# Kernel optimization log

Measured on AMD Instinct MI355X. Metric: run time of the kernel, lower is better.

Reference implementation:

```python
import jax, jax.numpy as jnp
import numpy as np
import math

NUM_HEADS = 12
HEAD_DIM = 64
DEGREE = 3
POLY_DIM = HEAD_DIM * (DEGREE + 1)  # 256
MEM_HID = 512
HIDDEN = 768


def setup_inputs() -> dict:
    key = jax.random.key(0)
    ks = jax.random.split(key, 6)
    B, S = 4, 2048
    hidden_states = jax.random.normal(ks[0], (B, S, HIDDEN), dtype=jnp.float32)
    # q projection weight stored (in, out) so y = x @ Wq
    Wq = jax.random.normal(ks[1], (HIDDEN, HIDDEN), dtype=jnp.float32) / np.sqrt(HIDDEN)
    # polynomial coefficients initialized to 1/i!
    coeffs = jnp.array([1.0 / math.factorial(i) for i in range(DEGREE + 1)], dtype=jnp.float32)
    # deep memory MLP: Linear(poly_dim->mem_hid) + ReLU + Linear(mem_hid->poly_dim)
    W1 = jax.random.normal(ks[2], (POLY_DIM, MEM_HID), dtype=jnp.float32) / np.sqrt(POLY_DIM)
    b1 = jnp.zeros((MEM_HID,), dtype=jnp.float32)
    W2 = jax.random.normal(ks[3], (MEM_HID, POLY_DIM), dtype=jnp.float32) / np.sqrt(MEM_HID)
    b2 = jnp.zeros((POLY_DIM,), dtype=jnp.float32)
    return {"hidden_states": hidden_states, "Wq": Wq, "coeffs": coeffs,
            "W1": W1, "b1": b1, "W2": W2, "b2": b2}


def _poly_map(x, coeffs):
    # x: [..., head_dim] -> [..., head_dim*(degree+1)]
    xs = jnp.clip(x, -10.0, 10.0)
    feats = [coeffs[0] * jnp.ones_like(x)]
    for i in range(1, DEGREE + 1):
        feats.append(jnp.clip(coeffs[i] * xs ** i, -1e6, 1e6))
    return jnp.concatenate(feats, axis=-1)


def reference(hidden_states, Wq, coeffs, W1, b1, W2, b2):
    B, S, H = hidden_states.shape
    # q projection -> [B, S, nh, hd]
    q = (hidden_states @ Wq).reshape(B, S, NUM_HEADS, HEAD_DIM)
    # polynomial feature expansion -> [B, S, nh, poly_dim]
    poly_q = _poly_map(q, coeffs)
    flat = poly_q.reshape(-1, POLY_DIM)  # [B*S*nh, poly_dim]
    # deep memory MLP (test-time memory read)
    h = jax.nn.relu(flat @ W1 + b1)
    mem = h @ W2 + b2  # [B*S*nh, poly_dim]
    # slice first head_dim dims, fold heads back into hidden
    out = mem[:, :HEAD_DIM].reshape(B, S, NUM_HEADS * HEAD_DIM)
    return out
```

## Files before the change

### kernel.cpp

```cpp
#include <hip/hip_runtime.h>


typedef unsigned short u16;
typedef __attribute__((ext_vector_type(8))) short short8;
typedef __attribute__((ext_vector_type(4))) float f32x4;
typedef __attribute__((ext_vector_type(4))) u16 u16x4;

__device__ __forceinline__ u16 f2bf(float f) {
    unsigned u = __builtin_bit_cast(unsigned, f);
    u += 0x7FFFu + ((u >> 16) & 1u);
    return (u16)(u >> 16);
}

__device__ __forceinline__ unsigned cvtpk_bf16(float lo, float hi) {
    unsigned r;
    asm("v_cvt_pk_bf16_f32 %0, %1, %2" : "=v"(r) : "v"(lo), "v"(hi));
    return r;
}

__device__ __forceinline__ void gl2lds16(const void* g, void* l) {
    __builtin_amdgcn_global_load_lds(
        (const __attribute__((address_space(1))) unsigned int*)g,
        (__attribute__((address_space(3))) unsigned int*)l, 16, 0, 0);
}

#define WAIT_VM_LGKM_BAR(N) \
    asm volatile("s_waitcnt vmcnt(" #N ") lgkmcnt(0)\n\ts_barrier" ::: "memory")
#define WAIT_LGKM_BAR() \
    asm volatile("s_waitcnt lgkmcnt(0)\n\ts_barrier" ::: "memory")

__global__ __launch_bounds__(256)
void prep(const float* __restrict__ X, u16* __restrict__ Xb,
          const float* __restrict__ Wq, u16* __restrict__ Wqb,
          const float* __restrict__ W1, u16* __restrict__ W1b,
          const float* __restrict__ W2, u16* __restrict__ W2b,
          const float* __restrict__ b1, const float* __restrict__ coeffs,
          float* __restrict__ b1e)
{
    __shared__ float t[32][33];
    const int b = blockIdx.x, tid = threadIdx.x;

    if (b < 6144) {
        const int i = b * 256 + tid;
        float4 v = reinterpret_cast<const float4*>(X)[i];
        u16x4 o = {f2bf(v.x), f2bf(v.y), f2bf(v.z), f2bf(v.w)};
        reinterpret_cast<u16x4*>(Xb)[i] = o;
    } else if (b < 6880) {
        const float* in; u16* out; int R, Cin, bx, by;
        int lb = b - 6144;
        if (lb < 576)      { in = Wq; out = Wqb; R = 768; Cin = 768; bx = lb % 24; by = lb / 24; }
        else if (lb < 704) { lb -= 576; in = W1; out = W1b; R = 256; Cin = 512; bx = lb % 16; by = lb / 16; }
        else               { lb -= 704; in = W2; out = W2b; R = 512; Cin = 256; bx = lb % 2;  by = lb / 2; }
        const int c0 = bx * 32, r0 = by * 32;
        const int tx = tid & 31, ty = tid >> 5;
        #pragma unroll
        for (int j = 0; j < 32; j += 8)
            t[ty + j][tx] = in[(size_t)(r0 + ty + j) * Cin + c0 + tx];
        __syncthreads();
        #pragma unroll
        for (int j = 0; j < 32; j += 8)
            out[(size_t)(c0 + ty + j) * R + r0 + tx] = f2bf(t[tx][ty + j]);
    } else {
        const int n = (b - 6880) * 256 + tid;
        float s = 0.f;
        #pragma unroll 8
        for (int k = 0; k < 64; ++k) s += W1[k * 512 + n];
        b1e[n] = b1[n] + coeffs[0] * s;
    }
}


__global__ __launch_bounds__(256, 2)
void fused(const u16* __restrict__ Xb, const u16* __restrict__ Wqb,
           const float* __restrict__ coeffs,
           const u16* __restrict__ W1t, const float* __restrict__ b1e,
           const u16* __restrict__ W2t, const float* __restrict__ b2,
           float* __restrict__ out)
{
    __shared__ u16 shm[37888];

    const int tid = threadIdx.x;
    const int w = tid >> 6, lane = tid & 63;
    const int lrow = lane >> 2, lslot = lane & 3;
    const int m16 = lane & 15, quad = lane >> 4;
    const int w0 = w & 1, w1 = w >> 1;
    const int tok0 = blockIdx.x * 64;
    const int bn = blockIdx.y * 128;
    const int h0 = blockIdx.y * 2;

    const float c1 = coeffs[1], c2 = coeffs[2], c3 = coeffs[3];

    u16* const qt    = shm;
    u16* const ring1 = shm + 9216;
    u16* const ring2 = shm + 9216;
    u16* const HsB   = shm + 21504;

    f32x4 acc[4][2];
    #pragma unroll
    for (int i = 0; i < 4; ++i)
        #pragma unroll
        for (int j = 0; j < 2; ++j)
            acc[i][j] = (f32x4){0.f, 0.f, 0.f, 0.f};

    auto stage1 = [&](int slot, int g) {
        const int k0 = g * 32;
        u16* Xs = ring1 + slot * 6144;
        u16* Ws = Xs + 2048;
        {
            const int row = w * 16 + lrow;
            const int cc = lslot ^ ((row >> 2) & 3);
            gl2lds16(Xb + (size_t)(tok0 + row) * 768 + k0 + cc * 8, &Xs[row * 32 + lslot * 8]);
        }
        #pragma unroll
        for (int i = 0; i < 2; ++i) {
            const int row = (w * 2 + i) * 16 + lrow;
            const int cc = lslot ^ ((row >> 2) & 3);
            gl2lds16(Wqb + (size_t)(bn + row) * 768 + k0 + cc * 8, &Ws[row * 32 + lslot * 8]);
        }
    };

    stage1(0, 0);
    stage1(1, 1);

    #pragma unroll 1
    for (int g = 0; g < 24; ++g) {
        WAIT_VM_LGKM_BAR(3);
        stage1((g + 2) % 3, (g + 2 <= 23) ? g + 2 : 23);
        const u16* Xs = ring1 + (g % 3) * 6144;
        const u16* Ws = Xs + 2048;
        short8 a[4], b[2];
        #pragma unroll
        for (int i = 0; i < 4; ++i) {
            const int row = w0 * 64 + i * 16 + m16;
            const int ss = quad ^ ((row >> 2) & 3);
            a[i] = *reinterpret_cast<const short8*>(&Ws[row * 32 + ss * 8]);
        }
        #pragma unroll
        for (int j = 0; j < 2; ++j) {
            const int row = w1 * 32 + j * 16 + m16;
            const int ss = quad ^ ((row >> 2) & 3);
            b[j] = *reinterpret_cast<const short8*>(&Xs[row * 32 + ss * 8]);
        }
        __builtin_amdgcn_s_setprio(1);
        #pragma unroll
        for (int i = 0; i < 4; ++i)
            #pragma unroll
            for (int j = 0; j < 2; ++j)
                acc[i][j] = __builtin_amdgcn_mfma_f32_16x16x32_bf16(a[i], b[j], acc[i][j], 0, 0, 0);
        __builtin_amdgcn_s_setprio(0);
    }

    asm volatile("s_waitcnt vmcnt(0) lgkmcnt(0)\n\ts_barrier" ::: "memory");

    #pragma unroll
    for (int i = 0; i < 4; ++i) {
        const int d0 = i * 16 + quad * 4;
        #pragma unroll
        for (int j = 0; j < 2; ++j) {
            const int l = (w1 * 32 + j * 16 + m16) * 2 + w0;
            float x0 = fminf(fmaxf(acc[i][j][0], -10.f), 10.f);
            float x1 = fminf(fmaxf(acc[i][j][1], -10.f), 10.f);
            float x2 = fminf(fmaxf(acc[i][j][2], -10.f), 10.f);
            float x3 = fminf(fmaxf(acc[i][j][3], -10.f), 10.f);
            uint2 v;
            v.x = cvtpk_bf16(x0, x1);
            v.y = cvtpk_bf16(x2, x3);
            *reinterpret_cast<uint2*>(&qt[l * 72 + d0]) = v;
        }
    }

    auto stage2 = [&](int slot, int g) {
        const int s = g / 6, c = g % 6;
        u16* W1s = ring2 + slot * 4096;
        #pragma unroll
        for (int i = 0; i < 2; ++i) {
            const int row = (w * 2 + i) * 16 + lrow;
            const int cc = lslot ^ ((row >> 2) & 3);
            gl2lds16(W1t + (size_t)(s * 128 + row) * 256 + 64 + c * 32 + cc * 8,
                     &W1s[row * 32 + lslot * 8]);
        }
    };
    auto stage2c = [&](int slot, int gg) {
        if (gg <= 23) stage2(slot, gg);
        else if (gg == 24) stage2(slot, 23);
    };

    short8 b3s[4][2];
    auto loadW2 = [&](int s) {
        #pragma unroll
        for (int c = 0; c < 4; ++c)
            #pragma unroll
            for (int j = 0; j < 2; ++j)
                b3s[c][j] = *reinterpret_cast<const short8*>(
                    W2t + (size_t)(w1 * 32 + j * 16 + m16) * 512 + s * 128 + c * 32 + quad * 8);
    };

    f32x4 accO[4][2];
    #pragma unroll
    for (int i = 0; i < 4; ++i)
        #pragma unroll
        for (int j = 0; j < 2; ++j)
            accO[i][j] = (f32x4){0.f, 0.f, 0.f, 0.f};

    stage2(0, 0);
    stage2(1, 1);

    #pragma unroll 1
    for (int s = 0; s < 4; ++s) {
        f32x4 accH[4][4];
        #pragma unroll
        for (int i = 0; i < 4; ++i)
            #pragma unroll
            for (int j = 0; j < 4; ++j)
                accH[i][j] = (f32x4){0.f, 0.f, 0.f, 0.f};

        auto computeH = [&](int slot, int c) {
            const u16* W1s = ring2 + slot * 4096;
            short8 af[4], bf[4];
            #pragma unroll
            for (int i = 0; i < 4; ++i) {
                const int row = w0 * 64 + i * 16 + m16;
                const int ss = quad ^ ((row >> 2) & 3);
                af[i] = *reinterpret_cast<const short8*>(&W1s[row * 32 + ss * 8]);
            }
            #pragma unroll
            for (int j = 0; j < 4; ++j) {
                const int row = w1 * 64 + j * 16 + m16;
                short8 qv = *reinterpret_cast<const short8*>(
                    &qt[row * 72 + (c & 1) * 32 + quad * 8]);
                float y[8];
                #pragma unroll
                for (int e = 0; e < 8; ++e) {
                    float x = __builtin_bit_cast(float, ((unsigned)(u16)qv[e]) << 16);
                    if (c < 2)      y[e] = c1 * x;
                    else if (c < 4) y[e] = c2 * (x * x);
                    else            y[e] = (c3 * (x * x)) * x;
                }
                uint4 pk;
                pk.x = cvtpk_bf16(y[0], y[1]);
                pk.y = cvtpk_bf16(y[2], y[3]);
                pk.z = cvtpk_bf16(y[4], y[5]);
                pk.w = cvtpk_bf16(y[6], y[7]);
                bf[j] = __builtin_bit_cast(short8, pk);
            }
            __builtin_amdgcn_s_setprio(1);
            #pragma unroll
            for (int i = 0; i < 4; ++i)
                #pragma unroll
                for (int j = 0; j < 4; ++j)
                    accH[i][j] = __builtin_amdgcn_mfma_f32_16x16x32_bf16(af[i], bf[j], accH[i][j], 0, 0, 0);
            __builtin_amdgcn_s_setprio(0);
        };

        const int g0 = s * 6;
        WAIT_VM_LGKM_BAR(2);  stage2c(2, g0 + 2); loadW2(s); computeH(0, 0);
        WAIT_VM_LGKM_BAR(10); stage2c(0, g0 + 3);            computeH(1, 1);
        WAIT_VM_LGKM_BAR(10); stage2c(1, g0 + 4);            computeH(2, 2);
        WAIT_VM_LGKM_BAR(2);  stage2c(2, g0 + 5);            computeH(0, 3);
        WAIT_VM_LGKM_BAR(2);  stage2c(0, g0 + 6);            computeH(1, 4);
        WAIT_VM_LGKM_BAR(2);  stage2c(1, g0 + 7);            computeH(2, 5);

        #pragma unroll
        for (int i = 0; i < 4; ++i) {
            const int lb = w0 * 64 + i * 16 + quad * 4;
            const f32x4 bv = *reinterpret_cast<const f32x4*>(&b1e[s * 128 + lb]);
            const int hc = lb >> 5;
            #pragma unroll
            for (int j = 0; j < 4; ++j) {
                const int tc = w1 * 64 + j * 16 + m16;
                const float h0v = fmaxf(accH[i][j][0] + bv[0], 0.f);
                const float h1v = fmaxf(accH[i][j][1] + bv[1], 0.f);
                const float h2v = fmaxf(accH[i][j][2] + bv[2], 0.f);
                const float h3v = fmaxf(accH[i][j][3] + bv[3], 0.f);
                uint2 v;
                v.x = cvtpk_bf16(h0v, h1v);
                v.y = cvtpk_bf16(h2v, h3v);
                const int sl = ((lb >> 3) & 3) ^ ((tc >> 2) & 3);
                *reinterpret_cast<uint2*>(&HsB[hc * 4096 + tc * 32 + sl * 8 + (lb & 7)]) = v;
            }
        }

        WAIT_LGKM_BAR();

        __builtin_amdgcn_s_setprio(1);
        #pragma unroll
        for (int c = 0; c < 4; ++c) {
            short8 a3[4];
            #pragma unroll
            for (int i = 0; i < 4; ++i) {
                const int tr = w0 * 64 + i * 16 + m16;
                const int ss = quad ^ ((tr >> 2) & 3);
                a3[i] = *reinterpret_cast<const short8*>(&HsB[c * 4096 + tr * 32 + ss * 8]);
            }
            #pragma unroll
            for (int i = 0; i < 4; ++i)
                #pragma unroll
                for (int j = 0; j < 2; ++j)
                    accO[i][j] = __builtin_amdgcn_mfma_f32_16x16x32_bf16(a3[i], b3s[c][j], accO[i][j], 0, 0, 0);
        }
        __builtin_amdgcn_s_setprio(0);
    }

    asm volatile("s_waitcnt vmcnt(0)" ::: "memory");

    #pragma unroll
    for (int j = 0; j < 2; ++j) {
        const int col = w1 * 32 + j * 16 + m16;
        const float bv = b2[col];
        #pragma unroll
        for (int i = 0; i < 4; ++i) {
            #pragma unroll
            for (int r = 0; r < 4; ++r) {
                const int l = w0 * 64 + i * 16 + quad * 4 + r;
                const size_t orow = (size_t)(tok0 + (l >> 1)) * 12 + h0 + (l & 1);
                out[orow * 64 + col] = accO[i][j][r] + bv;
            }
        }
    }
}


extern "C" void kernel_launch(void* const* d_in, const int* in_sizes, int n_in,
                              void* d_out, int out_size, void* d_ws, size_t ws_size,
                              hipStream_t stream) {
    const float* X      = (const float*)d_in[0];
    const float* Wq     = (const float*)d_in[1];
    const float* coeffs = (const float*)d_in[2];
    const float* W1     = (const float*)d_in[3];
    const float* b1     = (const float*)d_in[4];
    const float* W2     = (const float*)d_in[5];
    const float* b2     = (const float*)d_in[6];

    char* ws = (char*)d_ws;
    u16*   Xb  = (u16*)(ws);
    u16*   Wqb = (u16*)(ws + 12582912);
    u16*   W1b = (u16*)(ws + 13762560);
    u16*   W2b = (u16*)(ws + 14024704);
    float* b1e = (float*)(ws + 14090240);

    prep<<<6882, 256, 0, stream>>>(X, Xb, Wq, Wqb, W1, W1b, W2, W2b, b1, coeffs, b1e);

    fused<<<dim3(128, 6), 256, 0, stream>>>(Xb, Wqb, coeffs, W1b, b1e, W2b, b2,
                                            (float*)d_out);
}
```

Before: 151.0 us.

## Shrink LDS footprint to fit three blocks per CU in fused MLP kernel

Cuts shared memory from about 74KB to 52KB and raises launch bounds to three blocks per CU. To get there it drops the qt padding in favour of an XOR swizzle, shrinks the W1 ring from three slots to two with a full wait before each stage, and splits the hidden-activation buffer into two halves processed in sequence with extra barriers. The aim is more resident waves to hide latency. In exchange the prefetch pipeline gets shallower, barriers are added, and the tighter register budget may cause spills.

Result: slower. 186.0 us (+23.2%).

```diff
diff --git a/kernel.cpp b/kernel.cpp
--- a/kernel.cpp
+++ b/kernel.cpp
@@ -70,14 +70,14 @@
 }
 
 
-__global__ __launch_bounds__(256, 2)
+__global__ __launch_bounds__(256, 3)
 void fused(const u16* __restrict__ Xb, const u16* __restrict__ Wqb,
            const float* __restrict__ coeffs,
            const u16* __restrict__ W1t, const float* __restrict__ b1e,
            const u16* __restrict__ W2t, const float* __restrict__ b2,
            float* __restrict__ out)
 {
-    __shared__ u16 shm[37888];
+    __shared__ u16 shm[26624];
 
     const int tid = threadIdx.x;
     const int w = tid >> 6, lane = tid & 63;
@@ -91,9 +91,9 @@
     const float c1 = coeffs[1], c2 = coeffs[2], c3 = coeffs[3];
 
     u16* const qt    = shm;
-    u16* const ring1 = shm + 9216;
-    u16* const ring2 = shm + 9216;
-    u16* const HsB   = shm + 21504;
+    u16* const ring1 = shm + 8192;
+    u16* const ring2 = shm + 8192;
+    u16* const HsH   = shm + 16384;
 
     f32x4 acc[4][2];
     #pragma unroll
@@ -152,12 +152,26 @@
 
     asm volatile("s_waitcnt vmcnt(0) lgkmcnt(0)\n\ts_barrier" ::: "memory");
 
+    auto stage2 = [&](int slot, int g) {
+        const int s = g / 6, c = g % 6;
+        u16* W1s = ring2 + slot * 4096;
+        #pragma unroll
+        for (int i = 0; i < 2; ++i) {
+            const int row = (w * 2 + i) * 16 + lrow;
+            const int cc = lslot ^ ((row >> 2) & 3);
+            gl2lds16(W1t + (size_t)(s * 128 + row) * 256 + 64 + c * 32 + cc * 8,
+                     &W1s[row * 32 + lslot * 8]);
+        }
+    };
+    stage2(0, 0);
+
     #pragma unroll
     for (int i = 0; i < 4; ++i) {
-        const int d0 = i * 16 + quad * 4;
         #pragma unroll
         for (int j = 0; j < 2; ++j) {
             const int l = (w1 * 32 + j * 16 + m16) * 2 + w0;
+            const int d0 = i * 16 + quad * 4;
+            const int grp = (d0 >> 3) ^ ((l >> 1) & 7);
             float x0 = fminf(fmaxf(acc[i][j][0], -10.f), 10.f);
             float x1 = fminf(fmaxf(acc[i][j][1], -10.f), 10.f);
             float x2 = fminf(fmaxf(acc[i][j][2], -10.f), 10.f);
@@ -165,25 +179,9 @@
             uint2 v;
             v.x = cvtpk_bf16(x0, x1);
             v.y = cvtpk_bf16(x2, x3);
-            *reinterpret_cast<uint2*>(&qt[l * 72 + d0]) = v;
-        }
-    }
-
-    auto stage2 = [&](int slot, int g) {
-        const int s = g / 6, c = g % 6;
-        u16* W1s = ring2 + slot * 4096;
-        #pragma unroll
-        for (int i = 0; i < 2; ++i) {
-            const int row = (w * 2 + i) * 16 + lrow;
-            const int cc = lslot ^ ((row >> 2) & 3);
-            gl2lds16(W1t + (size_t)(s * 128 + row) * 256 + 64 + c * 32 + cc * 8,
-                     &W1s[row * 32 + lslot * 8]);
-        }
-    };
-    auto stage2c = [&](int slot, int gg) {
-        if (gg <= 23) stage2(slot, gg);
-        else if (gg == 24) stage2(slot, 23);
-    };
+            *reinterpret_cast<uint2*>(&qt[l * 64 + grp * 8 + (d0 & 7)]) = v;
+        }
+    }
 
     short8 b3s[4][2];
     auto loadW2 = [&](int s) {
@@ -202,9 +200,7 @@
         for (int j = 0; j < 2; ++j)
             accO[i][j] = (f32x4){0.f, 0.f, 0.f, 0.f};
 
-    stage2(0, 0);
-    stage2(1, 1);
-
+    int c = 0;
     #pragma unroll 1
     for (int s = 0; s < 4; ++s) {
         f32x4 accH[4][4];
@@ -214,8 +210,12 @@
             for (int j = 0; j < 4; ++j)
                 accH[i][j] = (f32x4){0.f, 0.f, 0.f, 0.f};
 
-        auto computeH = [&](int slot, int c) {
-            const u16* W1s = ring2 + slot * 4096;
+        #pragma unroll 1
+        for (int c6 = 0; c6 < 6; ++c6, ++c) {
+            WAIT_VM_LGKM_BAR(0);
+            if (c < 23) stage2((c + 1) & 1, c + 1);
+            if (c6 == 0) loadW2(s);
+            const u16* W1s = ring2 + (c & 1) * 4096;
             short8 af[4], bf[4];
             #pragma unroll
             for (int i = 0; i < 4; ++i) {
@@ -226,15 +226,15 @@
             #pragma unroll
             for (int j = 0; j < 4; ++j) {
                 const int row = w1 * 64 + j * 16 + m16;
-                short8 qv = *reinterpret_cast<const short8*>(
-                    &qt[row * 72 + (c & 1) * 32 + quad * 8]);
+                const int grp = ((c & 1) * 4 + quad) ^ ((row >> 1) & 7);
+                short8 qv = *reinterpret_cast<const short8*>(&qt[row * 64 + grp * 8]);
                 float y[8];
                 #pragma unroll
                 for (int e = 0; e < 8; ++e) {
                     float x = __builtin_bit_cast(float, ((unsigned)(u16)qv[e]) << 16);
-                    if (c < 2)      y[e] = c1 * x;
-                    else if (c < 4) y[e] = c2 * (x * x);
-                    else            y[e] = (c3 * (x * x)) * x;
+                    if (c6 < 2)      y[e] = c1 * x;
+                    else if (c6 < 4) y[e] = c2 * (x * x);
+                    else             y[e] = (c3 * (x * x)) * x;
                 }
                 uint4 pk;
                 pk.x = cvtpk_bf16(y[0], y[1]);
@@ -250,58 +250,54 @@
                 for (int j = 0; j < 4; ++j)
                     accH[i][j] = __builtin_amdgcn_mfma_f32_16x16x32_bf16(af[i], bf[j], accH[i][j], 0, 0, 0);
             __builtin_amdgcn_s_setprio(0);
-        };
-
-        const int g0 = s * 6;
-        WAIT_VM_LGKM_BAR(2);  stage2c(2, g0 + 2); loadW2(s); computeH(0, 0);
-        WAIT_VM_LGKM_BAR(10); stage2c(0, g0 + 3);            computeH(1, 1);
-        WAIT_VM_LGKM_BAR(10); stage2c(1, g0 + 4);            computeH(2, 2);
-        WAIT_VM_LGKM_BAR(2);  stage2c(2, g0 + 5);            computeH(0, 3);
-        WAIT_VM_LGKM_BAR(2);  stage2c(0, g0 + 6);            computeH(1, 4);
-        WAIT_VM_LGKM_BAR(2);  stage2c(1, g0 + 7);            computeH(2, 5);
-
-        #pragma unroll
-        for (int i = 0; i < 4; ++i) {
-            const int lb = w0 * 64 + i * 16 + quad * 4;
-            const f32x4 bv = *reinterpret_cast<const f32x4*>(&b1e[s * 128 + lb]);
-            const int hc = lb >> 5;
-            #pragma unroll
-            for (int j = 0; j < 4; ++j) {
-                const int tc = w1 * 64 + j * 16 + m16;
-                const float h0v = fmaxf(accH[i][j][0] + bv[0], 0.f);
-                const float h1v = fmaxf(accH[i][j][1] + bv[1], 0.f);
-                const float h2v = fmaxf(accH[i][j][2] + bv[2], 0.f);
-                const float h3v = fmaxf(accH[i][j][3] + bv[3], 0.f);
-                uint2 v;
-                v.x = cvtpk_bf16(h0v, h1v);
-                v.y = cvtpk_bf16(h2v, h3v);
-                const int sl = ((lb >> 3) & 3) ^ ((tc >> 2) & 3);
-                *reinterpret_cast<uint2*>(&HsB[hc * 4096 + tc * 32 + sl * 8 + (lb & 7)]) = v;
-            }
-        }
-
-        WAIT_LGKM_BAR();
-
-        __builtin_amdgcn_s_setprio(1);
-        #pragma unroll
-        for (int c = 0; c < 4; ++c) {
-            short8 a3[4];
-            #pragma unroll
-            for (int i = 0; i < 4; ++i) {
-                const int tr = w0 * 64 + i * 16 + m16;
-                const int ss = quad ^ ((tr >> 2) & 3);
-                a3[i] = *reinterpret_cast<const short8*>(&HsB[c * 4096 + tr * 32 + ss * 8]);
-            }
-            #pragma unroll
-            for (int i = 0; i < 4; ++i)
-                #pragma unroll
-                for (int j = 0; j < 2; ++j)
-                    accO[i][j] = __builtin_amdgcn_mfma_f32_16x16x32_bf16(a3[i], b3s[c][j], accO[i][j], 0, 0, 0);
-        }
-        __builtin_amdgcn_s_setprio(0);
-    }
-
-    asm volatile("s_waitcnt vmcnt(0)" ::: "memory");
+        }
+
+        #pragma unroll
+        for (int h = 0; h < 2; ++h) {
+            if (h == 1) { WAIT_LGKM_BAR(); }
+            if (w0 == h) {
+                #pragma unroll
+                for (int i = 0; i < 4; ++i) {
+                    const int lb = w0 * 64 + i * 16 + quad * 4;
+                    const f32x4 bv = *reinterpret_cast<const f32x4*>(&b1e[s * 128 + lb]);
+                    const int slot = (lb >> 5) & 1;
+                    #pragma unroll
+                    for (int j = 0; j < 4; ++j) {
+                        const int tc = w1 * 64 + j * 16 + m16;
+                        const float h0v = fmaxf(accH[i][j][0] + bv[0], 0.f);
+                        const float h1v = fmaxf(accH[i][j][1] + bv[1], 0.f);
+                        const float h2v = fmaxf(accH[i][j][2] + bv[2], 0.f);
+                        const float h3v = fmaxf(accH[i][j][3] + bv[3], 0.f);
+                        uint2 v;
+                        v.x = cvtpk_bf16(h0v, h1v);
+                        v.y = cvtpk_bf16(h2v, h3v);
+                        const int sl = ((lb >> 3) & 3) ^ ((tc >> 2) & 3);
+                        *reinterpret_cast<uint2*>(&HsH[slot * 4096 + tc * 32 + sl * 8 + (lb & 7)]) = v;
+                    }
+                }
+            }
+            WAIT_LGKM_BAR();
+
+            __builtin_amdgcn_s_setprio(1);
+            #pragma unroll
+            for (int c2 = 0; c2 < 2; ++c2) {
+                short8 a3[4];
+                #pragma unroll
+                for (int i = 0; i < 4; ++i) {
+                    const int tr = w0 * 64 + i * 16 + m16;
+                    const int ss = quad ^ ((tr >> 2) & 3);
+                    a3[i] = *reinterpret_cast<const short8*>(&HsH[c2 * 4096 + tr * 32 + ss * 8]);
+                }
+                #pragma unroll
+                for (int i = 0; i < 4; ++i)
+                    #pragma unroll
+                    for (int j = 0; j < 2; ++j)
+                        accO[i][j] = __builtin_amdgcn_mfma_f32_16x16x32_bf16(
+                            a3[i], b3s[h * 2 + c2][j], accO[i][j], 0, 0, 0);
+            }
+            __builtin_amdgcn_s_setprio(0);
+        }
+    }
 
     #pragma unroll
     for (int j = 0; j < 2; ++j) {
```

## Pair W1 chunks per barrier with 4-slot ring and XOR-swizzled q tile

Applied to the files above, without the earlier changes.

Restructures the stage-2 hidden-layer loop to process two K-chunks (one polynomial power) per barrier using a four-slot LDS ring, halving the number of barriers per hidden slice. The q tile drops its 72-element padded stride in favour of a 64-element stride with an XOR swizzle to avoid bank conflicts, and W1 prefetch is issued before the q epilogue so it overlaps that work. In exchange it uses more LDS, which could affect occupancy, and it carries more live registers per pair.

After: 149.9 us. No clear change (-0.7%).

```diff
diff --git a/kernel.cpp b/kernel.cpp
--- a/kernel.cpp
+++ b/kernel.cpp
@@ -77,7 +77,7 @@
            const u16* __restrict__ W2t, const float* __restrict__ b2,
            float* __restrict__ out)
 {
-    __shared__ u16 shm[37888];
+    __shared__ u16 shm[40960];
 
     const int tid = threadIdx.x;
     const int w = tid >> 6, lane = tid & 63;
@@ -91,9 +91,9 @@
     const float c1 = coeffs[1], c2 = coeffs[2], c3 = coeffs[3];
 
     u16* const qt    = shm;
-    u16* const ring1 = shm + 9216;
-    u16* const ring2 = shm + 9216;
-    u16* const HsB   = shm + 21504;
+    u16* const ring1 = shm + 8192;
+    u16* const ring2 = shm + 8192;
+    u16* const HsB   = shm + 24576;
 
     f32x4 acc[4][2];
     #pragma unroll
@@ -152,12 +152,31 @@
 
     asm volatile("s_waitcnt vmcnt(0) lgkmcnt(0)\n\ts_barrier" ::: "memory");
 
+    auto stage2 = [&](int slot, int g) {
+        const int sg = g / 6, cg = g % 6;
+        u16* W1s = ring2 + slot * 4096;
+        #pragma unroll
+        for (int i = 0; i < 2; ++i) {
+            const int row = (w * 2 + i) * 16 + lrow;
+            const int cc = lslot ^ ((row >> 2) & 3);
+            gl2lds16(W1t + (size_t)(sg * 128 + row) * 256 + 64 + cg * 32 + cc * 8,
+                     &W1s[row * 32 + lslot * 8]);
+        }
+    };
+    auto stage2c = [&](int slot, int gg) {
+        stage2(slot, (gg <= 23) ? gg : 23);
+    };
+
+    stage2(0, 0);
+    stage2(1, 1);
+
     #pragma unroll
     for (int i = 0; i < 4; ++i) {
-        const int d0 = i * 16 + quad * 4;
         #pragma unroll
         for (int j = 0; j < 2; ++j) {
             const int l = (w1 * 32 + j * 16 + m16) * 2 + w0;
+            const int d0 = i * 16 + quad * 4;
+            const int grp = (d0 >> 3) ^ ((l >> 1) & 7);
             float x0 = fminf(fmaxf(acc[i][j][0], -10.f), 10.f);
             float x1 = fminf(fmaxf(acc[i][j][1], -10.f), 10.f);
             float x2 = fminf(fmaxf(acc[i][j][2], -10.f), 10.f);
@@ -165,25 +184,9 @@
             uint2 v;
             v.x = cvtpk_bf16(x0, x1);
             v.y = cvtpk_bf16(x2, x3);
-            *reinterpret_cast<uint2*>(&qt[l * 72 + d0]) = v;
-        }
-    }
-
-    auto stage2 = [&](int slot, int g) {
-        const int s = g / 6, c = g % 6;
-        u16* W1s = ring2 + slot * 4096;
-        #pragma unroll
-        for (int i = 0; i < 2; ++i) {
-            const int row = (w * 2 + i) * 16 + lrow;
-            const int cc = lslot ^ ((row >> 2) & 3);
-            gl2lds16(W1t + (size_t)(s * 128 + row) * 256 + 64 + c * 32 + cc * 8,
-                     &W1s[row * 32 + lslot * 8]);
-        }
-    };
-    auto stage2c = [&](int slot, int gg) {
-        if (gg <= 23) stage2(slot, gg);
-        else if (gg == 24) stage2(slot, 23);
-    };
+            *reinterpret_cast<uint2*>(&qt[l * 64 + grp * 8 + (d0 & 7)]) = v;
+        }
+    }
 
     short8 b3s[4][2];
     auto loadW2 = [&](int s) {
@@ -202,9 +205,6 @@
         for (int j = 0; j < 2; ++j)
             accO[i][j] = (f32x4){0.f, 0.f, 0.f, 0.f};
 
-    stage2(0, 0);
-    stage2(1, 1);
-
     #pragma unroll 1
     for (int s = 0; s < 4; ++s) {
         f32x4 accH[4][4];
@@ -214,51 +214,63 @@
             for (int j = 0; j < 4; ++j)
                 accH[i][j] = (f32x4){0.f, 0.f, 0.f, 0.f};
 
-        auto computeH = [&](int slot, int c) {
-            const u16* W1s = ring2 + slot * 4096;
-            short8 af[4], bf[4];
+        auto computePair = [&](int slotA, int slotB, int pw) {
+            short8 afA[4], afB[4], bfA[4], bfB[4];
             #pragma unroll
             for (int i = 0; i < 4; ++i) {
                 const int row = w0 * 64 + i * 16 + m16;
                 const int ss = quad ^ ((row >> 2) & 3);
-                af[i] = *reinterpret_cast<const short8*>(&W1s[row * 32 + ss * 8]);
+                afA[i] = *reinterpret_cast<const short8*>(&ring2[slotA * 4096 + row * 32 + ss * 8]);
+                afB[i] = *reinterpret_cast<const short8*>(&ring2[slotB * 4096 + row * 32 + ss * 8]);
             }
             #pragma unroll
             for (int j = 0; j < 4; ++j) {
                 const int row = w1 * 64 + j * 16 + m16;
-                short8 qv = *reinterpret_cast<const short8*>(
-                    &qt[row * 72 + (c & 1) * 32 + quad * 8]);
-                float y[8];
+                const int sw = (row >> 1) & 7;
+                short8 qv0 = *reinterpret_cast<const short8*>(&qt[row * 64 + ((quad) ^ sw) * 8]);
+                short8 qv1 = *reinterpret_cast<const short8*>(&qt[row * 64 + ((4 + quad) ^ sw) * 8]);
+                float y0[8], y1[8];
                 #pragma unroll
                 for (int e = 0; e < 8; ++e) {
-                    float x = __builtin_bit_cast(float, ((unsigned)(u16)qv[e]) << 16);
-                    if (c < 2)      y[e] = c1 * x;
-                    else if (c < 4) y[e] = c2 * (x * x);
-                    else            y[e] = (c3 * (x * x)) * x;
+                    float xa = __builtin_bit_cast(float, ((unsigned)(u16)qv0[e]) << 16);
+                    float xb = __builtin_bit_cast(float, ((unsigned)(u16)qv1[e]) << 16);
+                    if (pw == 1)      { y0[e] = c1 * xa;             y1[e] = c1 * xb; }
+                    else if (pw == 2) { y0[e] = c2 * (xa * xa);      y1[e] = c2 * (xb * xb); }
+                    else              { y0[e] = (c3 * (xa * xa)) * xa; y1[e] = (c3 * (xb * xb)) * xb; }
                 }
-                uint4 pk;
-                pk.x = cvtpk_bf16(y[0], y[1]);
-                pk.y = cvtpk_bf16(y[2], y[3]);
-                pk.z = cvtpk_bf16(y[4], y[5]);
-                pk.w = cvtpk_bf16(y[6], y[7]);
-                bf[j] = __builtin_bit_cast(short8, pk);
+                uint4 pkA, pkB;
+                pkA.x = cvtpk_bf16(y0[0], y0[1]); pkA.y = cvtpk_bf16(y0[2], y0[3]);
+                pkA.z = cvtpk_bf16(y0[4], y0[5]); pkA.w = cvtpk_bf16(y0[6], y0[7]);
+                pkB.x = cvtpk_bf16(y1[0], y1[1]); pkB.y = cvtpk_bf16(y1[2], y1[3]);
+                pkB.z = cvtpk_bf16(y1[4], y1[5]); pkB.w = cvtpk_bf16(y1[6], y1[7]);
+                bfA[j] = __builtin_bit_cast(short8, pkA);
+                bfB[j] = __builtin_bit_cast(short8, pkB);
             }
             __builtin_amdgcn_s_setprio(1);
             #pragma unroll
             for (int i = 0; i < 4; ++i)
                 #pragma unroll
-                for (int j = 0; j < 4; ++j)
-                    accH[i][j] = __builtin_amdgcn_mfma_f32_16x16x32_bf16(af[i], bf[j], accH[i][j], 0, 0, 0);
+                for (int j = 0; j < 4; ++j) {
+                    accH[i][j] = __builtin_amdgcn_mfma_f32_16x16x32_bf16(afA[i], bfA[j], accH[i][j], 0, 0, 0);
+                    accH[i][j] = __builtin_amdgcn_mfma_f32_16x16x32_bf16(afB[i], bfB[j], accH[i][j], 0, 0, 0);
+                }
             __builtin_amdgcn_s_setprio(0);
         };
 
-        const int g0 = s * 6;
-        WAIT_VM_LGKM_BAR(2);  stage2c(2, g0 + 2); loadW2(s); computeH(0, 0);
-        WAIT_VM_LGKM_BAR(10); stage2c(0, g0 + 3);            computeH(1, 1);
-        WAIT_VM_LGKM_BAR(10); stage2c(1, g0 + 4);            computeH(2, 2);
-        WAIT_VM_LGKM_BAR(2);  stage2c(2, g0 + 5);            computeH(0, 3);
-        WAIT_VM_LGKM_BAR(2);  stage2c(0, g0 + 6);            computeH(1, 4);
-        WAIT_VM_LGKM_BAR(2);  stage2c(1, g0 + 7);            computeH(2, 5);
+        const int cb = s * 6;
+        WAIT_VM_LGKM_BAR(0);
+        stage2c((cb + 2) & 3, cb + 2);
+        stage2c((cb + 3) & 3, cb + 3);
+        loadW2(s);
+        computePair(cb & 3, (cb + 1) & 3, 1);
+        WAIT_VM_LGKM_BAR(8);
+        stage2c((cb + 4) & 3, cb + 4);
+        stage2c((cb + 5) & 3, cb + 5);
+        computePair((cb + 2) & 3, (cb + 3) & 3, 2);
+        WAIT_VM_LGKM_BAR(0);
+        stage2c((cb + 6) & 3, cb + 6);
+        stage2c((cb + 7) & 3, cb + 7);
+        computePair((cb + 4) & 3, (cb + 5) & 3, 3);
 
         #pragma unroll
         for (int i = 0; i < 4; ++i) {
```
